# Performance work log

Hardware: AMD Instinct MI355X
Metric: run time of the kernel (lower is better)

Reference implementation:

```python
import jax, jax.numpy as jnp
import numpy as np

N_NODES = 50000
N_EDGES = 800000
ND_IN, ED_IN, HID = 64, 64, 128


def setup_inputs() -> dict:
    key = jax.random.key(0)
    ks = jax.random.split(key, 14)
    s = 0.05
    return {
        "nfeats": jax.random.normal(ks[0], (N_NODES, ND_IN), dtype=jnp.float32),
        "efeats": jax.random.normal(ks[1], (N_EDGES, ED_IN), dtype=jnp.float32),
        # layer 1: W_apply in = ndim_in + ndim_in + edim = 192 -> 128; W_edge in = 2*128 -> 128
        "W1a_w": jax.random.normal(ks[2], (2 * ND_IN + ED_IN, HID), dtype=jnp.float32) * s,
        "W1a_b": jax.random.normal(ks[3], (HID,), dtype=jnp.float32) * s,
        "W1e_w": jax.random.normal(ks[4], (2 * HID, HID), dtype=jnp.float32) * s,
        "W1e_b": jax.random.normal(ks[5], (HID,), dtype=jnp.float32) * s,
        # layer 2: W_apply in = 128 + 128 + 128 = 384 -> 128; W_edge in = 256 -> 128
        "W2a_w": jax.random.normal(ks[6], (3 * HID, HID), dtype=jnp.float32) * s,
        "W2a_b": jax.random.normal(ks[7], (HID,), dtype=jnp.float32) * s,
        "W2e_w": jax.random.normal(ks[8], (2 * HID, HID), dtype=jnp.float32) * s,
        "W2e_b": jax.random.normal(ks[9], (HID,), dtype=jnp.float32) * s,
        "u": jax.random.randint(ks[10], (N_EDGES,), 0, N_NODES, dtype=jnp.int32),
        "v": jax.random.randint(ks[11], (N_EDGES,), 0, N_NODES, dtype=jnp.int32),
    }


def _layer(hn, he, u, v, Wa_w, Wa_b, We_w, We_b, n_nodes):
    # message: concat(src node feats, edge feats), mean-reduced onto dst nodes
    msg = jnp.concatenate([hn[u], he], axis=1)                      # [E, nd+ed]
    msum = jax.ops.segment_sum(msg, v, num_segments=n_nodes)        # [N, nd+ed]
    deg = jax.ops.segment_sum(jnp.ones((v.shape[0],), msg.dtype), v,
                              num_segments=n_nodes)                  # [N]
    h_neigh = msum / jnp.maximum(deg, 1.0)[:, None]                  # zero-degree -> 0
    hn_new = jax.nn.relu(jnp.concatenate([hn, h_neigh], axis=1) @ Wa_w + Wa_b)
    e_in = jnp.concatenate([hn_new[u], hn_new[v]], axis=1)           # [E, 2*nd_out]
    he_new = jax.nn.relu(e_in @ We_w + We_b)
    return hn_new, he_new


def reference(nfeats, efeats, W1a_w, W1a_b, W1e_w, W1e_b,
              W2a_w, W2a_b, W2e_w, W2e_b, u, v):
    n_nodes = nfeats.shape[0]
    hn, he = _layer(nfeats, efeats, u, v, W1a_w, W1a_b, W1e_w, W1e_b, n_nodes)
    hn, he = _layer(hn, he, u, v, W2a_w, W2a_b, W2e_w, W2e_b, n_nodes)
    return hn, he
```

## Files before the change

kernel.cpp:

```cpp
#include <hip/hip_runtime.h>

#define NN 50000
#define NE 800000

typedef __attribute__((ext_vector_type(8))) short short8;
typedef __attribute__((ext_vector_type(4))) float floatx4;

__device__ __forceinline__ unsigned short f2b(float f){
  unsigned u = __float_as_uint(f);
  u += 0x7fffu + ((u >> 16) & 1u);
  return (unsigned short)(u >> 16);
}
__device__ __forceinline__ float blo(unsigned u){ return __uint_as_float(u << 16); }
__device__ __forceinline__ float bhi(unsigned u){ return __uint_as_float(u & 0xffff0000u); }

#define NB_NF   3125
#define NB_HIST 3125
#define NB_W1A  96
#define NB_W1E  128
#define NB_W2A  192
#define NB_W2E  128

__global__ __launch_bounds__(256) void k_prep(const float* __restrict__ nf,
                                              const float* __restrict__ W1a,
                                              const float* __restrict__ W1e,
                                              const float* __restrict__ W2a,
                                              const float* __restrict__ W2e,
                                              const int* __restrict__ v,
                                              unsigned short* __restrict__ nfb,
                                              unsigned short* __restrict__ w1as,
                                              unsigned short* __restrict__ w1es,
                                              unsigned short* __restrict__ w2as,
                                              unsigned short* __restrict__ w2es,
                                              int* __restrict__ cnt){
  int b = blockIdx.x, t = threadIdx.x;
  if(b < NB_NF){
    int i = b * 256 + t;
    float4 vv = ((const float4*)nf)[i];
    unsigned a = (unsigned)f2b(vv.x) | ((unsigned)f2b(vv.y) << 16);
    unsigned c = (unsigned)f2b(vv.z) | ((unsigned)f2b(vv.w) << 16);
    ((uint2*)nfb)[i] = make_uint2(a, c);
  } else if(b < NB_NF + NB_HIST){
    int e = (b - NB_NF) * 256 + t;
    if(e < NE) atomicAdd(&cnt[v[e]], 1);
  } else if(b < NB_NF + NB_HIST + NB_W1A){
    int i = (b - NB_NF - NB_HIST) * 256 + t;
    int k = i >> 7, n = i & 127;
    w1as[((k >> 5) * 128 + n) * 32 + (k & 31)] = f2b(W1a[i]);
  } else if(b < NB_NF + NB_HIST + NB_W1A + NB_W1E){
    int i = (b - NB_NF - NB_HIST - NB_W1A) * 256 + t;
    int k = i >> 8, n = i & 255;
    float val = W1e[(size_t)(k + ((n >> 7) << 7)) * 128 + (n & 127)];
    w1es[((k >> 5) * 256 + n) * 32 + (k & 31)] = f2b(val);
  } else if(b < NB_NF + NB_HIST + NB_W1A + NB_W1E + NB_W2A){
    int i = (b - NB_NF - NB_HIST - NB_W1A - NB_W1E) * 256 + t;
    int k = i >> 7, n = i & 127;
    w2as[((k >> 5) * 128 + n) * 32 + (k & 31)] = f2b(W2a[i]);
  } else {
    int i = (b - NB_NF - NB_HIST - NB_W1A - NB_W1E - NB_W2A) * 256 + t;
    int k = i >> 8, n = i & 255;
    float val = W2e[(size_t)(k + ((n >> 7) << 7)) * 128 + (n & 127)];
    w2es[((k >> 5) * 256 + n) * 32 + (k & 31)] = f2b(val);
  }
}

__global__ __launch_bounds__(512) void k_scanA(const int* __restrict__ cnt,
                                               int* __restrict__ rowptr,
                                               int* __restrict__ part){
  __shared__ int lds[512];
  int t = threadIdx.x;
  int i = blockIdx.x * 512 + t;
  int x = (i < NN) ? cnt[i] : 0;
  lds[t] = x;
  __syncthreads();
  for(int o = 1; o < 512; o <<= 1){
    int y = (t >= o) ? lds[t - o] : 0;
    __syncthreads();
    lds[t] += y;
    __syncthreads();
  }
  if(i < NN) rowptr[i] = lds[t] - x;
  if(t == 511) part[blockIdx.x] = lds[511];
}

__global__ void k_scanB(int* __restrict__ part, int* __restrict__ rowptr){
  if(threadIdx.x == 0 && blockIdx.x == 0){
    int run = 0;
    for(int b = 0; b < 98; b++){ int tt = part[b]; part[b] = run; run += tt; }
    rowptr[NN] = run;
  }
}

__global__ __launch_bounds__(512) void k_scanC(int* __restrict__ rowptr,
                                               const int* __restrict__ part,
                                               int* __restrict__ cursor){
  int i = blockIdx.x * 512 + threadIdx.x;
  if(i < NN){
    int val = rowptr[i] + part[blockIdx.x];
    rowptr[i] = val;
    cursor[i] = val;
  }
}

__global__ __launch_bounds__(256) void k_fill(const int* __restrict__ u, const int* __restrict__ v,
                                              int* __restrict__ cursor, int2* __restrict__ ebuf){
  int e = blockIdx.x * 256 + threadIdx.x;
  if(e < NE){
    int pos = atomicAdd(&cursor[v[e]], 1);
    ebuf[pos] = make_int2(u[e], e);
  }
}

__global__ __launch_bounds__(256) void k_agg1(const int* __restrict__ rowptr,
                                              const int2* __restrict__ ebuf,
                                              const unsigned short* __restrict__ nfb,
                                              const float* __restrict__ ef,
                                              unsigned short* __restrict__ hneigh1){
  int node = blockIdx.x * 4 + (threadIdx.x >> 6);
  int l = threadIdx.x & 63;
  int beg = rowptr[node], end = rowptr[node + 1];
  bool sel = l >= 32;
  int cn = 2 * l;
  int ce = 2 * (l - 32);
  float a0 = 0.f, a1 = 0.f;
  int i = beg;
  for(; i + 4 <= end; i += 4){
    int2 e0 = ebuf[i], e1 = ebuf[i + 1], e2 = ebuf[i + 2], e3 = ebuf[i + 3];
    if(sel){
      float2 t0 = *(const float2*)(ef + (size_t)((unsigned)e0.y * 64u) + ce);
      float2 t1 = *(const float2*)(ef + (size_t)((unsigned)e1.y * 64u) + ce);
      float2 t2 = *(const float2*)(ef + (size_t)((unsigned)e2.y * 64u) + ce);
      float2 t3 = *(const float2*)(ef + (size_t)((unsigned)e3.y * 64u) + ce);
      a0 += t0.x + t1.x + t2.x + t3.x;
      a1 += t0.y + t1.y + t2.y + t3.y;
    } else {
      unsigned t0 = *(const unsigned*)(nfb + (size_t)((unsigned)e0.x * 64u) + cn);
      unsigned t1 = *(const unsigned*)(nfb + (size_t)((unsigned)e1.x * 64u) + cn);
      unsigned t2 = *(const unsigned*)(nfb + (size_t)((unsigned)e2.x * 64u) + cn);
      unsigned t3 = *(const unsigned*)(nfb + (size_t)((unsigned)e3.x * 64u) + cn);
      a0 += blo(t0) + blo(t1) + blo(t2) + blo(t3);
      a1 += bhi(t0) + bhi(t1) + bhi(t2) + bhi(t3);
    }
  }
  for(; i < end; i++){
    int2 e = ebuf[i];
    if(sel){
      float2 t = *(const float2*)(ef + (size_t)((unsigned)e.y * 64u) + ce);
      a0 += t.x; a1 += t.y;
    } else {
      unsigned t = *(const unsigned*)(nfb + (size_t)((unsigned)e.x * 64u) + cn);
      a0 += blo(t); a1 += bhi(t);
    }
  }
  float inv = 1.f / fmaxf((float)(end - beg), 1.f);
  unsigned o = (unsigned)f2b(a0 * inv) | ((unsigned)f2b(a1 * inv) << 16);
  *(unsigned*)(hneigh1 + (size_t)node * 128 + 2 * l) = o;
}

__global__ __launch_bounds__(256) void k_agg2(const int* __restrict__ rowptr,
                                              const int2* __restrict__ ebuf,
                                              const unsigned short* __restrict__ hn1,
                                              const unsigned short* __restrict__ PQ1,
                                              const float* __restrict__ b1e,
                                              unsigned short* __restrict__ hneigh2){
  int node = blockIdx.x * 4 + (threadIdx.x >> 6);
  int l = threadIdx.x & 63;
  int beg = rowptr[node], end = rowptr[node + 1];
  bool sel = l >= 32;
  int c4 = sel ? 4 * (l - 32) : 4 * l;
  const unsigned short* base = sel ? (PQ1 + c4) : (hn1 + c4);
  unsigned stride = sel ? 256u : 128u;
  float q0 = 0.f, q1 = 0.f, q2 = 0.f, q3 = 0.f, fl = -__builtin_inff();
  if(sel){
    uint2 qq = *(const uint2*)(PQ1 + (size_t)node * 256 + 128 + c4);
    q0 = blo(qq.x) + b1e[c4];
    q1 = bhi(qq.x) + b1e[c4 + 1];
    q2 = blo(qq.y) + b1e[c4 + 2];
    q3 = bhi(qq.y) + b1e[c4 + 3];
    fl = 0.f;
  }
  const int* eb = (const int*)ebuf;
  float a0 = 0.f, a1 = 0.f, a2 = 0.f, a3 = 0.f;
  int i = beg;
  for(; i + 4 <= end; i += 4){
    unsigned s0 = (unsigned)eb[2 * i];
    unsigned s1 = (unsigned)eb[2 * i + 2];
    unsigned s2 = (unsigned)eb[2 * i + 4];
    unsigned s3 = (unsigned)eb[2 * i + 6];
    uint2 t0 = *(const uint2*)(base + (size_t)(s0 * stride));
    uint2 t1 = *(const uint2*)(base + (size_t)(s1 * stride));
    uint2 t2 = *(const uint2*)(base + (size_t)(s2 * stride));
    uint2 t3 = *(const uint2*)(base + (size_t)(s3 * stride));
    a0 += fmaxf(blo(t0.x) + q0, fl) + fmaxf(blo(t1.x) + q0, fl)
        + fmaxf(blo(t2.x) + q0, fl) + fmaxf(blo(t3.x) + q0, fl);
    a1 += fmaxf(bhi(t0.x) + q1, fl) + fmaxf(bhi(t1.x) + q1, fl)
        + fmaxf(bhi(t2.x) + q1, fl) + fmaxf(bhi(t3.x) + q1, fl);
    a2 += fmaxf(blo(t0.y) + q2, fl) + fmaxf(blo(t1.y) + q2, fl)
        + fmaxf(blo(t2.y) + q2, fl) + fmaxf(blo(t3.y) + q2, fl);
    a3 += fmaxf(bhi(t0.y) + q3, fl) + fmaxf(bhi(t1.y) + q3, fl)
        + fmaxf(bhi(t2.y) + q3, fl) + fmaxf(bhi(t3.y) + q3, fl);
  }
  for(; i < end; i++){
    unsigned s = (unsigned)eb[2 * i];
    uint2 t = *(const uint2*)(base + (size_t)(s * stride));
    a0 += fmaxf(blo(t.x) + q0, fl);
    a1 += fmaxf(bhi(t.x) + q1, fl);
    a2 += fmaxf(blo(t.y) + q2, fl);
    a3 += fmaxf(bhi(t.y) + q3, fl);
  }
  float inv = 1.f / fmaxf((float)(end - beg), 1.f);
  unsigned o0 = (unsigned)f2b(a0 * inv) | ((unsigned)f2b(a1 * inv) << 16);
  unsigned o1 = (unsigned)f2b(a2 * inv) | ((unsigned)f2b(a3 * inv) << 16);
  *(uint2*)(hneigh2 + (size_t)node * 256 + 4 * l) = make_uint2(o0, o1);
}

__global__ __launch_bounds__(256) void k_he2(const int* __restrict__ u, const int* __restrict__ v,
                                             const unsigned short* __restrict__ PQ2,
                                             const float* __restrict__ b2e,
                                             float* __restrict__ outp){
  int idx = blockIdx.x * 256 + threadIdx.x;
  int e = idx >> 5;
  if(e >= NE) return;
  int c = (idx & 31) * 4;
  int uu = u[e], vv = v[e];
  uint2 p = *(const uint2*)(PQ2 + (size_t)uu * 256 + c);
  uint2 q = *(const uint2*)(PQ2 + (size_t)vv * 256 + 128 + c);
  float4 b = *(const float4*)(b2e + c);
  float4 r;
  r.x = fmaxf(blo(p.x) + blo(q.x) + b.x, 0.f);
  r.y = fmaxf(bhi(p.x) + bhi(q.x) + b.y, 0.f);
  r.z = fmaxf(blo(p.y) + blo(q.y) + b.z, 0.f);
  r.w = fmaxf(bhi(p.y) + bhi(q.y) + b.w, 0.f);
  *(float4*)(outp + (size_t)e * 128 + c) = r;
}

template<int K, int N, bool BR, int OM>
__global__ __launch_bounds__(256) void k_gemm(const unsigned short* __restrict__ A0, int W0,
                                              const unsigned short* __restrict__ A1, int W1,
                                              const unsigned short* __restrict__ Bs,
                                              const float* __restrict__ bias,
                                              float* __restrict__ Cf,
                                              unsigned short* __restrict__ Cb){
  constexpr int KT = K / 32;
  const int nb = blockIdx.y;
  const int wid = threadIdx.x >> 6, lane = threadIdx.x & 63;
  const int ln = lane & 15, kg = lane >> 4;
  const int r0 = blockIdx.x * 128 + wid * 32;
  int r_[2];
  r_[0] = min(r0 + ln, NN - 1);
  r_[1] = min(r0 + 16 + ln, NN - 1);

  floatx4 acc[2][8];
#pragma unroll
  for(int a = 0; a < 2; a++)
#pragma unroll
    for(int b = 0; b < 8; b++) acc[a][b] = (floatx4){0.f, 0.f, 0.f, 0.f};

#pragma unroll
  for(int kt = 0; kt < KT; kt++){
    int k = kt * 32 + kg * 8;
    short8 af[2];
#pragma unroll
    for(int mt = 0; mt < 2; mt++){
      const unsigned short* p = (k < W0) ? (A0 + (size_t)r_[mt] * W0 + k)
                                         : (A1 + (size_t)r_[mt] * W1 + (k - W0));
      af[mt] = *(const short8*)p;
    }
    const unsigned short* bp = Bs + ((size_t)(kt * N + nb * 128)) * 32 + kg * 8;
#pragma unroll
    for(int nt = 0; nt < 8; nt++){
      short8 bfrag = *(const short8*)(bp + (nt * 16 + ln) * 32);
      acc[0][nt] = __builtin_amdgcn_mfma_f32_16x16x32_bf16(af[0], bfrag, acc[0][nt], 0, 0, 0);
      acc[1][nt] = __builtin_amdgcn_mfma_f32_16x16x32_bf16(af[1], bfrag, acc[1][nt], 0, 0, 0);
    }
  }
#pragma unroll
  for(int mt = 0; mt < 2; mt++){
    int rb = r0 + mt * 16 + kg * 4;
#pragma unroll
    for(int nt = 0; nt < 8; nt++){
      int col = nb * 128 + nt * 16 + ln;
      float bv = BR ? bias[col] : 0.f;
#pragma unroll
      for(int rr = 0; rr < 4; rr++){
        int row = rb + rr;
        if(row < NN){
          float vv = acc[mt][nt][rr];
          if(BR) vv = fmaxf(vv + bv, 0.f);
          if(OM == 0 || OM == 2) Cf[(size_t)row * N + col] = vv;
          if(OM == 1 || OM == 2) Cb[(size_t)row * N + col] = f2b(vv);
        }
      }
    }
  }
}

extern "C" void kernel_launch(void* const* d_in, const int* in_sizes, int n_in,
                              void* d_out, int out_size, void* d_ws, size_t ws_size,
                              hipStream_t stream){
  const float* nf  = (const float*)d_in[0];
  const float* ef  = (const float*)d_in[1];
  const float* W1a = (const float*)d_in[2];
  const float* b1a = (const float*)d_in[3];
  const float* W1e = (const float*)d_in[4];
  const float* b1e = (const float*)d_in[5];
  const float* W2a = (const float*)d_in[6];
  const float* b2a = (const float*)d_in[7];
  const float* W2e = (const float*)d_in[8];
  const float* b2e = (const float*)d_in[9];
  const int*   u   = (const int*)d_in[10];
  const int*   v   = (const int*)d_in[11];

  char* ws = (char*)d_ws;
  int* rowptr = (int*)(ws + 0);
  int* cnt    = (int*)(ws + 0x40000);
  int* part   = (int*)(ws + 0x80000);
  unsigned short* w1as = (unsigned short*)(ws + 0x90000);
  unsigned short* w1es = (unsigned short*)(ws + 0xA0000);
  unsigned short* w2as = (unsigned short*)(ws + 0xC0000);
  unsigned short* w2es = (unsigned short*)(ws + 0xE0000);
  unsigned short* nfb  = (unsigned short*)(ws + (size_t)(1u   << 20));
  int2*           ebuf = (int2*)          (ws + (size_t)(8u   << 20));
  unsigned short* hn1b = (unsigned short*)(ws + (size_t)(15u  << 20));
  unsigned short* hn2b = (unsigned short*)(ws + (size_t)(28u  << 20));
  unsigned short* PQ   = (unsigned short*)(ws + (size_t)(41u  << 20));
  unsigned short* hnb1 = (unsigned short*)(ws + (size_t)(67u  << 20));
  unsigned short* hnb2 = (unsigned short*)(ws + (size_t)(80u  << 20));

  hipMemsetAsync(ws + 0x40000, 0, 0x40200, stream);

  k_prep<<<NB_NF + NB_HIST + NB_W1A + NB_W1E + NB_W2A + NB_W2E, 256, 0, stream>>>(
      nf, W1a, W1e, W2a, W2e, v, nfb, w1as, w1es, w2as, w2es, cnt);

  k_scanA<<<98, 512, 0, stream>>>(cnt, rowptr, part);
  k_scanB<<<1,  64,  0, stream>>>(part, rowptr);
  k_scanC<<<98, 512, 0, stream>>>(rowptr, part, cnt);
  k_fill <<<3125, 256, 0, stream>>>(u, v, cnt, ebuf);

  k_agg1<<<12500, 256, 0, stream>>>(rowptr, ebuf, nfb, ef, hnb1);
  k_gemm<192, 128, true,  1><<<dim3(391, 1), 256, 0, stream>>>(nfb, 64, hnb1, 128, w1as, b1a, nullptr, hn1b);
  k_gemm<128, 256, false, 1><<<dim3(391, 2), 256, 0, stream>>>(hn1b, 128, hn1b, 128, w1es, nullptr, nullptr, PQ);

  k_agg2<<<12500, 256, 0, stream>>>(rowptr, ebuf, hn1b, PQ, b1e, hnb2);
  k_gemm<384, 128, true,  2><<<dim3(391, 1), 256, 0, stream>>>(hn1b, 128, hnb2, 256, w2as, b2a, (float*)d_out, hn2b);
  k_gemm<128, 256, false, 1><<<dim3(391, 2), 256, 0, stream>>>(hn2b, 128, hn2b, 128, w2es, nullptr, nullptr, PQ);
  k_he2<<<100000, 256, 0, stream>>>(u, v, PQ, b2e, (float*)d_out + (size_t)NN * 128);
}
```

Measured before the change: 942.9 us.

## Widen gather loads in aggregation kernels and halve GEMM row tile

The aggregation kernels now split each wavefront into two half-waves that process alternate edges. Each lane loads wider vectors (8 or 16 bytes instead of 4 or 8), and the two halves are combined with a cross-lane shuffle at the end. The edge-output kernel gives each thread 8 columns with 16-byte loads, and the GEMM drops from 32 rows per wave to 16, doubling the grid. The aim is fewer, wider memory transactions in the gather-bound kernels and more parallelism in the GEMMs, at the cost of extra shuffles and less B-fragment reuse per wave.

```diff
diff --git a/kernel.cpp b/kernel.cpp
--- a/kernel.cpp
+++ b/kernel.cpp
@@ -118,43 +118,67 @@
                                               unsigned short* __restrict__ hneigh1){
   int node = blockIdx.x * 4 + (threadIdx.x >> 6);
   int l = threadIdx.x & 63;
+  int h = l >> 5;
+  int g = l & 31;
+  bool sel = g >= 16;
   int beg = rowptr[node], end = rowptr[node + 1];
-  bool sel = l >= 32;
-  int cn = 2 * l;
-  int ce = 2 * (l - 32);
-  float a0 = 0.f, a1 = 0.f;
+  const unsigned short* nbase = nfb + 4 * g;
+  const float* ebase = ef + 4 * (g - 16);
+  float a0 = 0.f, a1 = 0.f, a2 = 0.f, a3 = 0.f;
   int i = beg;
-  for(; i + 4 <= end; i += 4){
-    int2 e0 = ebuf[i], e1 = ebuf[i + 1], e2 = ebuf[i + 2], e3 = ebuf[i + 3];
+  for(; i + 8 <= end; i += 8){
+    int2 e0 = ebuf[i + h], e1 = ebuf[i + 2 + h], e2 = ebuf[i + 4 + h], e3 = ebuf[i + 6 + h];
     if(sel){
-      float2 t0 = *(const float2*)(ef + (size_t)((unsigned)e0.y * 64u) + ce);
-      float2 t1 = *(const float2*)(ef + (size_t)((unsigned)e1.y * 64u) + ce);
-      float2 t2 = *(const float2*)(ef + (size_t)((unsigned)e2.y * 64u) + ce);
-      float2 t3 = *(const float2*)(ef + (size_t)((unsigned)e3.y * 64u) + ce);
+      float4 t0 = *(const float4*)(ebase + (size_t)((unsigned)e0.y) * 64u);
+      float4 t1 = *(const float4*)(ebase + (size_t)((unsigned)e1.y) * 64u);
+      float4 t2 = *(const float4*)(ebase + (size_t)((unsigned)e2.y) * 64u);
+      float4 t3 = *(const float4*)(ebase + (size_t)((unsigned)e3.y) * 64u);
       a0 += t0.x + t1.x + t2.x + t3.x;
       a1 += t0.y + t1.y + t2.y + t3.y;
+      a2 += t0.z + t1.z + t2.z + t3.z;
+      a3 += t0.w + t1.w + t2.w + t3.w;
     } else {
-      unsigned t0 = *(const unsigned*)(nfb + (size_t)((unsigned)e0.x * 64u) + cn);
-      unsigned t1 = *(const unsigned*)(nfb + (size_t)((unsigned)e1.x * 64u) + cn);
-      unsigned t2 = *(const unsigned*)(nfb + (size_t)((unsigned)e2.x * 64u) + cn);
-      unsigned t3 = *(const unsigned*)(nfb + (size_t)((unsigned)e3.x * 64u) + cn);
-      a0 += blo(t0) + blo(t1) + blo(t2) + blo(t3);
-      a1 += bhi(t0) + bhi(t1) + bhi(t2) + bhi(t3);
+      uint2 t0 = *(const uint2*)(nbase + (size_t)((unsigned)e0.x) * 64u);
+      uint2 t1 = *(const uint2*)(nbase + (size_t)((unsigned)e1.x) * 64u);
+      uint2 t2 = *(const uint2*)(nbase + (size_t)((unsigned)e2.x) * 64u);
+      uint2 t3 = *(const uint2*)(nbase + (size_t)((unsigned)e3.x) * 64u);
+      a0 += blo(t0.x) + blo(t1.x) + blo(t2.x) + blo(t3.x);
+      a1 += bhi(t0.x) + bhi(t1.x) + bhi(t2.x) + bhi(t3.x);
+      a2 += blo(t0.y) + blo(t1.y) + blo(t2.y) + blo(t3.y);
+      a3 += bhi(t0.y) + bhi(t1.y) + bhi(t2.y) + bhi(t3.y);
     }
   }
-  for(; i < end; i++){
+  for(; i + 2 <= end; i += 2){
+    int2 e = ebuf[i + h];
+    if(sel){
+      float4 t = *(const float4*)(ebase + (size_t)((unsigned)e.y) * 64u);
+      a0 += t.x; a1 += t.y; a2 += t.z; a3 += t.w;
+    } else {
+      uint2 t = *(const uint2*)(nbase + (size_t)((unsigned)e.x) * 64u);
+      a0 += blo(t.x); a1 += bhi(t.x); a2 += blo(t.y); a3 += bhi(t.y);
+    }
+  }
+  if(h == 0 && i < end){
     int2 e = ebuf[i];
     if(sel){
-      float2 t = *(const float2*)(ef + (size_t)((unsigned)e.y * 64u) + ce);
-      a0 += t.x; a1 += t.y;
+      float4 t = *(const float4*)(ebase + (size_t)((unsigned)e.y) * 64u);
+      a0 += t.x; a1 += t.y; a2 += t.z; a3 += t.w;
     } else {
-      unsigned t = *(const unsigned*)(nfb + (size_t)((unsigned)e.x * 64u) + cn);
-      a0 += blo(t); a1 += bhi(t);
+      uint2 t = *(const uint2*)(nbase + (size_t)((unsigned)e.x) * 64u);
+      a0 += blo(t.x); a1 += bhi(t.x); a2 += blo(t.y); a3 += bhi(t.y);
     }
   }
-  float inv = 1.f / fmaxf((float)(end - beg), 1.f);
-  unsigned o = (unsigned)f2b(a0 * inv) | ((unsigned)f2b(a1 * inv) << 16);
-  *(unsigned*)(hneigh1 + (size_t)node * 128 + 2 * l) = o;
+  a0 += __shfl_xor(a0, 32);
+  a1 += __shfl_xor(a1, 32);
+  a2 += __shfl_xor(a2, 32);
+  a3 += __shfl_xor(a3, 32);
+  if(h == 0){
+    float inv = 1.f / fmaxf((float)(end - beg), 1.f);
+    unsigned o0 = (unsigned)f2b(a0 * inv) | ((unsigned)f2b(a1 * inv) << 16);
+    unsigned o1 = (unsigned)f2b(a2 * inv) | ((unsigned)f2b(a3 * inv) << 16);
+    int c = sel ? (64 + 4 * (g - 16)) : (4 * g);
+    *(uint2*)(hneigh1 + (size_t)node * 128 + c) = make_uint2(o0, o1);
+  }
 }
 
 __global__ __launch_bounds__(256) void k_agg2(const int* __restrict__ rowptr,
@@ -165,53 +189,93 @@
                                               unsigned short* __restrict__ hneigh2){
   int node = blockIdx.x * 4 + (threadIdx.x >> 6);
   int l = threadIdx.x & 63;
+  int h = l >> 5;
+  int g = l & 31;
+  bool sel = g >= 16;
   int beg = rowptr[node], end = rowptr[node + 1];
-  bool sel = l >= 32;
-  int c4 = sel ? 4 * (l - 32) : 4 * l;
-  const unsigned short* base = sel ? (PQ1 + c4) : (hn1 + c4);
+  int c8 = sel ? 8 * (g - 16) : 8 * g;
+  const unsigned short* base = sel ? (PQ1 + c8) : (hn1 + c8);
   unsigned stride = sel ? 256u : 128u;
-  float q0 = 0.f, q1 = 0.f, q2 = 0.f, q3 = 0.f, fl = -__builtin_inff();
+  float q[8];
+  float fl = -__builtin_inff();
+#pragma unroll
+  for(int j = 0; j < 8; j++) q[j] = 0.f;
   if(sel){
-    uint2 qq = *(const uint2*)(PQ1 + (size_t)node * 256 + 128 + c4);
-    q0 = blo(qq.x) + b1e[c4];
-    q1 = bhi(qq.x) + b1e[c4 + 1];
-    q2 = blo(qq.y) + b1e[c4 + 2];
-    q3 = bhi(qq.y) + b1e[c4 + 3];
+    uint4 qq = *(const uint4*)(PQ1 + (size_t)node * 256 + 128 + c8);
+    float4 b0 = *(const float4*)(b1e + c8);
+    float4 b1 = *(const float4*)(b1e + c8 + 4);
+    q[0] = blo(qq.x) + b0.x; q[1] = bhi(qq.x) + b0.y;
+    q[2] = blo(qq.y) + b0.z; q[3] = bhi(qq.y) + b0.w;
+    q[4] = blo(qq.z) + b1.x; q[5] = bhi(qq.z) + b1.y;
+    q[6] = blo(qq.w) + b1.z; q[7] = bhi(qq.w) + b1.w;
     fl = 0.f;
   }
   const int* eb = (const int*)ebuf;
-  float a0 = 0.f, a1 = 0.f, a2 = 0.f, a3 = 0.f;
+  float a[8];
+#pragma unroll
+  for(int j = 0; j < 8; j++) a[j] = 0.f;
   int i = beg;
-  for(; i + 4 <= end; i += 4){
-    unsigned s0 = (unsigned)eb[2 * i];
-    unsigned s1 = (unsigned)eb[2 * i + 2];
-    unsigned s2 = (unsigned)eb[2 * i + 4];
-    unsigned s3 = (unsigned)eb[2 * i + 6];
-    uint2 t0 = *(const uint2*)(base + (size_t)(s0 * stride));
-    uint2 t1 = *(const uint2*)(base + (size_t)(s1 * stride));
-    uint2 t2 = *(const uint2*)(base + (size_t)(s2 * stride));
-    uint2 t3 = *(const uint2*)(base + (size_t)(s3 * stride));
-    a0 += fmaxf(blo(t0.x) + q0, fl) + fmaxf(blo(t1.x) + q0, fl)
-        + fmaxf(blo(t2.x) + q0, fl) + fmaxf(blo(t3.x) + q0, fl);
-    a1 += fmaxf(bhi(t0.x) + q1, fl) + fmaxf(bhi(t1.x) + q1, fl)
-        + fmaxf(bhi(t2.x) + q1, fl) + fmaxf(bhi(t3.x) + q1, fl);
-    a2 += fmaxf(blo(t0.y) + q2, fl) + fmaxf(blo(t1.y) + q2, fl)
-        + fmaxf(blo(t2.y) + q2, fl) + fmaxf(blo(t3.y) + q2, fl);
-    a3 += fmaxf(bhi(t0.y) + q3, fl) + fmaxf(bhi(t1.y) + q3, fl)
-        + fmaxf(bhi(t2.y) + q3, fl) + fmaxf(bhi(t3.y) + q3, fl);
-  }
-  for(; i < end; i++){
+  for(; i + 8 <= end; i += 8){
+    unsigned s0 = (unsigned)eb[2 * (i + h)];
+    unsigned s1 = (unsigned)eb[2 * (i + 2 + h)];
+    unsigned s2 = (unsigned)eb[2 * (i + 4 + h)];
+    unsigned s3 = (unsigned)eb[2 * (i + 6 + h)];
+    uint4 t0 = *(const uint4*)(base + (size_t)(s0 * stride));
+    uint4 t1 = *(const uint4*)(base + (size_t)(s1 * stride));
+    uint4 t2 = *(const uint4*)(base + (size_t)(s2 * stride));
+    uint4 t3 = *(const uint4*)(base + (size_t)(s3 * stride));
+    a[0] += fmaxf(blo(t0.x) + q[0], fl) + fmaxf(blo(t1.x) + q[0], fl)
+          + fmaxf(blo(t2.x) + q[0], fl) + fmaxf(blo(t3.x) + q[0], fl);
+    a[1] += fmaxf(bhi(t0.x) + q[1], fl) + fmaxf(bhi(t1.x) + q[1], fl)
+          + fmaxf(bhi(t2.x) + q[1], fl) + fmaxf(bhi(t3.x) + q[1], fl);
+    a[2] += fmaxf(blo(t0.y) + q[2], fl) + fmaxf(blo(t1.y) + q[2], fl)
+          + fmaxf(blo(t2.y) + q[2], fl) + fmaxf(blo(t3.y) + q[2], fl);
+    a[3] += fmaxf(bhi(t0.y) + q[3], fl) + fmaxf(bhi(t1.y) + q[3], fl)
+          + fmaxf(bhi(t2.y) + q[3], fl) + fmaxf(bhi(t3.y) + q[3], fl);
+    a[4] += fmaxf(blo(t0.z) + q[4], fl) + fmaxf(blo(t1.z) + q[4], fl)
+          + fmaxf(blo(t2.z) + q[4], fl) + fmaxf(blo(t3.z) + q[4], fl);
+    a[5] += fmaxf(bhi(t0.z) + q[5], fl) + fmaxf(bhi(t1.z) + q[5], fl)
+          + fmaxf(bhi(t2.z) + q[5], fl) + fmaxf(bhi(t3.z) + q[5], fl);
+    a[6] += fmaxf(blo(t0.w) + q[6], fl) + fmaxf(blo(t1.w) + q[6], fl)
+          + fmaxf(blo(t2.w) + q[6], fl) + fmaxf(blo(t3.w) + q[6], fl);
+    a[7] += fmaxf(bhi(t0.w) + q[7], fl) + fmaxf(bhi(t1.w) + q[7], fl)
+          + fmaxf(bhi(t2.w) + q[7], fl) + fmaxf(bhi(t3.w) + q[7], fl);
+  }
+  for(; i + 2 <= end; i += 2){
+    unsigned s = (unsigned)eb[2 * (i + h)];
+    uint4 t = *(const uint4*)(base + (size_t)(s * stride));
+    a[0] += fmaxf(blo(t.x) + q[0], fl);
+    a[1] += fmaxf(bhi(t.x) + q[1], fl);
+    a[2] += fmaxf(blo(t.y) + q[2], fl);
+    a[3] += fmaxf(bhi(t.y) + q[3], fl);
+    a[4] += fmaxf(blo(t.z) + q[4], fl);
+    a[5] += fmaxf(bhi(t.z) + q[5], fl);
+    a[6] += fmaxf(blo(t.w) + q[6], fl);
+    a[7] += fmaxf(bhi(t.w) + q[7], fl);
+  }
+  if(h == 0 && i < end){
     unsigned s = (unsigned)eb[2 * i];
-    uint2 t = *(const uint2*)(base + (size_t)(s * stride));
-    a0 += fmaxf(blo(t.x) + q0, fl);
-    a1 += fmaxf(bhi(t.x) + q1, fl);
-    a2 += fmaxf(blo(t.y) + q2, fl);
-    a3 += fmaxf(bhi(t.y) + q3, fl);
-  }
-  float inv = 1.f / fmaxf((float)(end - beg), 1.f);
-  unsigned o0 = (unsigned)f2b(a0 * inv) | ((unsigned)f2b(a1 * inv) << 16);
-  unsigned o1 = (unsigned)f2b(a2 * inv) | ((unsigned)f2b(a3 * inv) << 16);
-  *(uint2*)(hneigh2 + (size_t)node * 256 + 4 * l) = make_uint2(o0, o1);
+    uint4 t = *(const uint4*)(base + (size_t)(s * stride));
+    a[0] += fmaxf(blo(t.x) + q[0], fl);
+    a[1] += fmaxf(bhi(t.x) + q[1], fl);
+    a[2] += fmaxf(blo(t.y) + q[2], fl);
+    a[3] += fmaxf(bhi(t.y) + q[3], fl);
+    a[4] += fmaxf(blo(t.z) + q[4], fl);
+    a[5] += fmaxf(bhi(t.z) + q[5], fl);
+    a[6] += fmaxf(blo(t.w) + q[6], fl);
+    a[7] += fmaxf(bhi(t.w) + q[7], fl);
+  }
+#pragma unroll
+  for(int j = 0; j < 8; j++) a[j] += __shfl_xor(a[j], 32);
+  if(h == 0){
+    float inv = 1.f / fmaxf((float)(end - beg), 1.f);
+    unsigned o0 = (unsigned)f2b(a[0] * inv) | ((unsigned)f2b(a[1] * inv) << 16);
+    unsigned o1 = (unsigned)f2b(a[2] * inv) | ((unsigned)f2b(a[3] * inv) << 16);
+    unsigned o2 = (unsigned)f2b(a[4] * inv) | ((unsigned)f2b(a[5] * inv) << 16);
+    unsigned o3 = (unsigned)f2b(a[6] * inv) | ((unsigned)f2b(a[7] * inv) << 16);
+    int c = sel ? (128 + 8 * (g - 16)) : (8 * g);
+    *(uint4*)(hneigh2 + (size_t)node * 256 + c) = make_uint4(o0, o1, o2, o3);
+  }
 }
 
 __global__ __launch_bounds__(256) void k_he2(const int* __restrict__ u, const int* __restrict__ v,
@@ -219,19 +283,25 @@
                                              const float* __restrict__ b2e,
                                              float* __restrict__ outp){
   int idx = blockIdx.x * 256 + threadIdx.x;
-  int e = idx >> 5;
+  int e = idx >> 4;
   if(e >= NE) return;
-  int c = (idx & 31) * 4;
+  int c = (idx & 15) * 8;
   int uu = u[e], vv = v[e];
-  uint2 p = *(const uint2*)(PQ2 + (size_t)uu * 256 + c);
-  uint2 q = *(const uint2*)(PQ2 + (size_t)vv * 256 + 128 + c);
-  float4 b = *(const float4*)(b2e + c);
-  float4 r;
-  r.x = fmaxf(blo(p.x) + blo(q.x) + b.x, 0.f);
-  r.y = fmaxf(bhi(p.x) + bhi(q.x) + b.y, 0.f);
-  r.z = fmaxf(blo(p.y) + blo(q.y) + b.z, 0.f);
-  r.w = fmaxf(bhi(p.y) + bhi(q.y) + b.w, 0.f);
-  *(float4*)(outp + (size_t)e * 128 + c) = r;
+  uint4 p = *(const uint4*)(PQ2 + (size_t)uu * 256 + c);
+  uint4 q = *(const uint4*)(PQ2 + (size_t)vv * 256 + 128 + c);
+  float4 b0 = *(const float4*)(b2e + c);
+  float4 b1 = *(const float4*)(b2e + c + 4);
+  float4 r0, r1;
+  r0.x = fmaxf(blo(p.x) + blo(q.x) + b0.x, 0.f);
+  r0.y = fmaxf(bhi(p.x) + bhi(q.x) + b0.y, 0.f);
+  r0.z = fmaxf(blo(p.y) + blo(q.y) + b0.z, 0.f);
+  r0.w = fmaxf(bhi(p.y) + bhi(q.y) + b0.w, 0.f);
+  r1.x = fmaxf(blo(p.z) + blo(q.z) + b1.x, 0.f);
+  r1.y = fmaxf(bhi(p.z) + bhi(q.z) + b1.y, 0.f);
+  r1.z = fmaxf(blo(p.w) + blo(q.w) + b1.z, 0.f);
+  r1.w = fmaxf(bhi(p.w) + bhi(q.w) + b1.w, 0.f);
+  *(float4*)(outp + (size_t)e * 128 + c) = r0;
+  *(float4*)(outp + (size_t)e * 128 + c + 4) = r1;
 }
 
 template<int K, int N, bool BR, int OM>
@@ -245,51 +315,39 @@
   const int nb = blockIdx.y;
   const int wid = threadIdx.x >> 6, lane = threadIdx.x & 63;
   const int ln = lane & 15, kg = lane >> 4;
-  const int r0 = blockIdx.x * 128 + wid * 32;
-  int r_[2];
-  r_[0] = min(r0 + ln, NN - 1);
-  r_[1] = min(r0 + 16 + ln, NN - 1);
-
-  floatx4 acc[2][8];
-#pragma unroll
-  for(int a = 0; a < 2; a++)
-#pragma unroll
-    for(int b = 0; b < 8; b++) acc[a][b] = (floatx4){0.f, 0.f, 0.f, 0.f};
+  const int r0 = blockIdx.x * 64 + wid * 16;
+  int r = min(r0 + ln, NN - 1);
+
+  floatx4 acc[8];
+#pragma unroll
+  for(int b = 0; b < 8; b++) acc[b] = (floatx4){0.f, 0.f, 0.f, 0.f};
 
 #pragma unroll
   for(int kt = 0; kt < KT; kt++){
     int k = kt * 32 + kg * 8;
-    short8 af[2];
-#pragma unroll
-    for(int mt = 0; mt < 2; mt++){
-      const unsigned short* p = (k < W0) ? (A0 + (size_t)r_[mt] * W0 + k)
-                                         : (A1 + (size_t)r_[mt] * W1 + (k - W0));
-      af[mt] = *(const short8*)p;
-    }
+    const unsigned short* p = (k < W0) ? (A0 + (size_t)r * W0 + k)
+                                       : (A1 + (size_t)r * W1 + (k - W0));
+    short8 af = *(const short8*)p;
     const unsigned short* bp = Bs + ((size_t)(kt * N + nb * 128)) * 32 + kg * 8;
 #pragma unroll
     for(int nt = 0; nt < 8; nt++){
       short8 bfrag = *(const short8*)(bp + (nt * 16 + ln) * 32);
-      acc[0][nt] = __builtin_amdgcn_mfma_f32_16x16x32_bf16(af[0], bfrag, acc[0][nt], 0, 0, 0);
-      acc[1][nt] = __builtin_amdgcn_mfma_f32_16x16x32_bf16(af[1], bfrag, acc[1][nt], 0, 0, 0);
+      acc[nt] = __builtin_amdgcn_mfma_f32_16x16x32_bf16(af, bfrag, acc[nt], 0, 0, 0);
     }
   }
-#pragma unroll
-  for(int mt = 0; mt < 2; mt++){
-    int rb = r0 + mt * 16 + kg * 4;
-#pragma unroll
-    for(int nt = 0; nt < 8; nt++){
-      int col = nb * 128 + nt * 16 + ln;
-      float bv = BR ? bias[col] : 0.f;
-#pragma unroll
-      for(int rr = 0; rr < 4; rr++){
-        int row = rb + rr;
-        if(row < NN){
-          float vv = acc[mt][nt][rr];
-          if(BR) vv = fmaxf(vv + bv, 0.f);
-          if(OM == 0 || OM == 2) Cf[(size_t)row * N + col] = vv;
-          if(OM == 1 || OM == 2) Cb[(size_t)row * N + col] = f2b(vv);
-        }
+  int rb = r0 + kg * 4;
+#pragma unroll
+  for(int nt = 0; nt < 8; nt++){
+    int col = nb * 128 + nt * 16 + ln;
+    float bv = BR ? bias[col] : 0.f;
+#pragma unroll
+    for(int rr = 0; rr < 4; rr++){
+      int row = rb + rr;
+      if(row < NN){
+        float vv = acc[nt][rr];
+        if(BR) vv = fmaxf(vv + bv, 0.f);
+        if(OM == 0 || OM == 2) Cf[(size_t)row * N + col] = vv;
+        if(OM == 1 || OM == 2) Cb[(size_t)row * N + col] = f2b(vv);
       }
     }
   }
@@ -338,11 +396,11 @@
   k_fill <<<3125, 256, 0, stream>>>(u, v, cnt, ebuf);
 
   k_agg1<<<12500, 256, 0, stream>>>(rowptr, ebuf, nfb, ef, hnb1);
-  k_gemm<192, 128, true,  1><<<dim3(391, 1), 256, 0, stream>>>(nfb, 64, hnb1, 128, w1as, b1a, nullptr, hn1b);
-  k_gemm<128, 256, false, 1><<<dim3(391, 2), 256, 0, stream>>>(hn1b, 128, hn1b, 128, w1es, nullptr, nullptr, PQ);
+  k_gemm<192, 128, true,  1><<<dim3(782, 1), 256, 0, stream>>>(nfb, 64, hnb1, 128, w1as, b1a, nullptr, hn1b);
+  k_gemm<128, 256, false, 1><<<dim3(782, 2), 256, 0, stream>>>(hn1b, 128, hn1b, 128, w1es, nullptr, nullptr, PQ);
 
   k_agg2<<<12500, 256, 0, stream>>>(rowptr, ebuf, hn1b, PQ, b1e, hnb2);
-  k_gemm<384, 128, true,  2><<<dim3(391, 1), 256, 0, stream>>>(hn1b, 128, hnb2, 256, w2as, b2a, (float*)d_out, hn2b);
-  k_gemm<128, 256, false, 1><<<dim3(391, 2), 256, 0, stream>>>(hn2b, 128, hn2b, 128, w2es, nullptr, nullptr, PQ);
-  k_he2<<<100000, 256, 0, stream>>>(u, v, PQ, b2e, (float*)d_out + (size_t)NN * 128);
-}
+  k_gemm<384, 128, true,  2><<<dim3(782, 1), 256, 0, stream>>>(hn1b, 128, hnb2, 256, w2as, b2a, (float*)d_out, hn2b);
+  k_gemm<128, 256, false, 1><<<dim3(782, 2), 256, 0, stream>>>(hn2b, 128, hn2b, 128, w2es, nullptr, nullptr, PQ);
+  k_he2<<<50000, 256, 0, stream>>>(u, v, PQ, b2e, (float*)d_out + (size_t)NN * 128);
+}
```

Result: faster. 920.3 us (-2.4%).
